# Performance work log

Measured on AMD Instinct MI355X. Metric: run time of the kernel, lower is better.

The kernel has to match this reference:

```python
import jax, jax.numpy as jnp
import numpy as np

B, S, IN, H, D, NH, L, C = 32, 512, 3, 64, 128, 8, 4, 5
NSUB = 10          # euler substeps per interval: dt = interval/10 for these inputs
MAX_CONSEC = 50    # max_consecutive_steps in torch code
DH = D // NH
EPS = 1e-5


def _ln(x, g, b):
    m = x.mean(-1, keepdims=True)
    v = ((x - m) ** 2).mean(-1, keepdims=True)
    return (x - m) / jnp.sqrt(v + EPS) * g + b


def setup_inputs():
    key = jax.random.key(0)
    ks = jax.random.split(key, 24)
    def g(i, shape, scale=0.05):
        return jax.random.normal(ks[i], shape, dtype=jnp.float32) * scale
    dts = jax.random.uniform(ks[0], (B, S), minval=0.001, maxval=0.05, dtype=jnp.float32)
    times = jnp.cumsum(dts, axis=1)  # strictly increasing, positive
    return dict(
        time_series=jax.random.normal(ks[1], (B, S, IN), dtype=jnp.float32),
        times=times,
        noise=jax.random.normal(ks[2], (S, NSUB, B, H), dtype=jnp.float32),
        mask=jnp.ones((B, S), dtype=bool),
        enc_w=g(3, (IN, H)), enc_b=jnp.zeros((H,)),
        enc_g=jnp.ones((H,)), enc_beta=jnp.zeros((H,)),
        dw1=g(4, (H + 1, 2 * H)), db1=jnp.zeros((2 * H,)),
        dw2=g(5, (2 * H, H)), db2=jnp.zeros((H,)),
        dw3=g(6, (H, H)), db3=jnp.zeros((H,)),
        aw1=g(7, (1, H)), ab1=jnp.zeros((H,)),
        aw2=g(8, (H, H)), ab2=jnp.zeros((H,)),
        bw1=g(9, (1, H)), bb1=jnp.zeros((H,)),
        bw2=g(10, (H, H)), bb2=jnp.zeros((H,)),
        min_diff=jnp.float32(0.1),
        in_w=g(11, (H, D)), in_b=jnp.zeros((D,)),
        wq=g(12, (L, D, D)), bq=jnp.zeros((L, D)),
        wk=g(13, (L, D, D)), bk=jnp.zeros((L, D)),
        wv=g(14, (L, D, D)), bv=jnp.zeros((L, D)),
        wo=g(15, (L, D, D)), bo=jnp.zeros((L, D)),
        ln1_g=jnp.ones((L, D)), ln1_b=jnp.zeros((L, D)),
        ln2_g=jnp.ones((L, D)), ln2_b=jnp.zeros((L, D)),
        fw1=g(16, (L, D, 4 * D)), fb1=jnp.zeros((L, 4 * D)),
        fw2=g(17, (L, 4 * D, D)), fb2=jnp.zeros((L, D)),
        cw1=g(18, (D, D // 2)), cb1=jnp.zeros((D // 2,)),
        cw2=g(19, (D // 2, C)), cb2=jnp.zeros((C,)),
    )


def reference(time_series, times, noise, mask, enc_w, enc_b, enc_g, enc_beta,
              dw1, db1, dw2, db2, dw3, db3, aw1, ab1, aw2, ab2, bw1, bb1, bw2, bb2,
              min_diff, in_w, in_b, wq, bq, wk, bk, wv, bv, wo, bo,
              ln1_g, ln1_b, ln2_g, ln2_b, fw1, fb1, fw2, fb2, cw1, cb1, cw2, cb2):
    # feature encoder: Linear -> LayerNorm -> ReLU (dropout off / eval)
    enc = jax.nn.relu(_ln(time_series @ enc_w + enc_b, enc_g, enc_beta))  # (B,S,H)

    def drift(t, y):
        tcol = jnp.full((y.shape[0], 1), t, dtype=y.dtype)
        ty = jnp.concatenate([y, tcol], axis=1)
        h1 = jnp.tanh(ty @ dw1 + db1)
        h2 = jnp.tanh(h1 @ dw2 + db2)
        return h2 @ dw3 + db3

    def diffusion(t, y):
        tcol = jnp.full((y.shape[0], 1), t, dtype=y.dtype)
        A = jax.nn.softplus(jnp.tanh(tcol @ aw1 + ab1) @ aw2 + ab2)
        Bt = jnp.tanh(jnp.tanh(tcol @ bw1 + bb1) @ bw2 + bb2)
        return A + Bt * y + jnp.abs(min_diff)

    t_seq = times[0]  # torch code uses batch element 0's timestamps for sdeint

    def step(carry, xs):
        state, consec = carry
        enc_i, t_prev, t_cur, dW = xs  # dW: (NSUB,B,H) standard normals
        h = (t_cur - t_prev) / NSUB    # dt = interval/10 (< self.dt for these inputs)
        sqh = jnp.sqrt(h)
        y0 = jax.lax.stop_gradient(state)  # torch detaches y0 at every step

        def sub(y, kw):
            k, dw = kw
            t = t_prev + k * h
            return y + drift(t, y) * h + diffusion(t, y) * sqh * dw, None

        y_int, _ = jax.lax.scan(sub, y0, (jnp.arange(NSUB, dtype=jnp.float32), dW))
        skip = consec >= MAX_CONSEC
        out = jnp.where(skip, enc_i, y_int)
        consec = jnp.where(skip, jnp.int32(0), consec + 1)
        return (out, consec), out

    y0 = enc[:, 0]
    xs = (jnp.swapaxes(enc, 0, 1)[1:], t_seq[:-1], t_seq[1:], noise[1:])
    _, traj = jax.lax.scan(step, (y0, jnp.int32(0)), xs)
    sde_features = jnp.concatenate([y0[:, None], jnp.swapaxes(traj, 0, 1)], axis=1)  # (B,S,H)

    mf = mask.astype(sde_features.dtype)
    sde_features = sde_features * mf[..., None]  # MaskedSequenceProcessor.apply_mask

    # ContiFormer (post-LN transformer encoder) over SDE features
    x = sde_features @ in_w + in_b  # (B,S,D)
    neg = jnp.asarray(-1e9, x.dtype)
    for l in range(L):
        q = (x @ wq[l] + bq[l]).reshape(B, S, NH, DH)
        k = (x @ wk[l] + bk[l]).reshape(B, S, NH, DH)
        v = (x @ wv[l] + bv[l]).reshape(B, S, NH, DH)
        scores = jnp.einsum('bqhd,bkhd->bhqk', q, k) / np.float32(np.sqrt(DH))
        scores = jnp.where(mask[:, None, None, :], scores, neg)
        att = jax.nn.softmax(scores, axis=-1)
        o = jnp.einsum('bhqk,bkhd->bqhd', att, v).reshape(B, S, D) @ wo[l] + bo[l]
        x = _ln(x + o, ln1_g[l], ln1_b[l])
        f = jax.nn.relu(x @ fw1[l] + fb1[l]) @ fw2[l] + fb2[l]
        x = _ln(x + f, ln2_g[l], ln2_b[l])
    pooled = (x * mf[..., None]).sum(1) / jnp.maximum(mf.sum(1, keepdims=True), 1.0)

    logits = jax.nn.relu(pooled @ cw1 + cb1) @ cw2 + cb2
    return logits, sde_features
```

## Files before the change

kernel.cpp:

```cpp
#include <hip/hip_runtime.h>
#include <hip/hip_bf16.h>


typedef __attribute__((ext_vector_type(8))) short short8;
typedef __attribute__((ext_vector_type(4))) float f32x4;

static constexpr int OFF_TS      = 0;
static constexpr int OFF_TIMES   = 49152;
static constexpr int OFF_ENCW    = 65536;
static constexpr int OFF_ENCB    = 65728;
static constexpr int OFF_ENCG    = 65792;
static constexpr int OFF_ENCBETA = 65856;
static constexpr int OFF_DW1     = 65920;
static constexpr int OFF_DB1     = 74240;
static constexpr int OFF_DW2     = 74368;
static constexpr int OFF_DB2     = 82560;
static constexpr int OFF_DW3     = 82624;
static constexpr int OFF_DB3     = 86720;
static constexpr int OFF_AW1     = 86784;
static constexpr int OFF_AB1     = 86848;
static constexpr int OFF_AW2     = 86912;
static constexpr int OFF_AB2     = 91008;
static constexpr int OFF_BW1     = 91072;
static constexpr int OFF_BB1     = 91136;
static constexpr int OFF_BW2     = 91200;
static constexpr int OFF_BB2     = 95296;
static constexpr int OFF_MD      = 95360;
static constexpr int OFF_INW     = 95424;
static constexpr int OFF_INB     = 103616;
static constexpr int OFF_WQ      = 103744;
static constexpr int OFF_BQ      = 169280;
static constexpr int OFF_WK      = 169792;
static constexpr int OFF_BK      = 235328;
static constexpr int OFF_WV      = 235840;
static constexpr int OFF_BV      = 301376;
static constexpr int OFF_WO      = 301888;
static constexpr int OFF_BO      = 367424;
static constexpr int OFF_LN1G    = 367936;
static constexpr int OFF_LN1B    = 368448;
static constexpr int OFF_LN2G    = 368960;
static constexpr int OFF_LN2B    = 369472;
static constexpr int OFF_FW1     = 369984;
static constexpr int OFF_FB1     = 632128;
static constexpr int OFF_FW2     = 634176;
static constexpr int OFF_FB2     = 896320;
static constexpr int OFF_CW1     = 896832;
static constexpr int OFF_CB1     = 905024;
static constexpr int OFF_CW2     = 905088;
static constexpr int OFF_CB2     = 905472;
static constexpr int OFF_FLAG    = 905536;
static constexpr int OFF_ENC     = 905600;
static constexpr int OFF_COEFA   = 3002752;
static constexpr int OFF_COEFB   = 3329792;
static constexpr int OFF_B1C     = 3656832;
static constexpr int OFF_X       = 4310912;
static constexpr int OFF_XBF     = 6408064;
static constexpr int OFF_QKVBF   = 7456640;
static constexpr int OFF_OBF     = 10602368;
static constexpr int OFF_HBF     = 11650944;
static constexpr int OFF_SDEBF   = 15845248;
static constexpr int OFF_WQKVT   = 16369536;
static constexpr int OFF_WOT     = 16467840;
static constexpr int OFF_FW1T    = 16500608;
static constexpr int OFF_FW2T    = 16631680;
static constexpr int OFF_INWT    = 16762752;
static constexpr int OFF_BQKV    = 16766848;
static constexpr int OFF_TMP     = 23185280;

struct PtrPack { const void* p[45]; };

__device__ inline float wsum64(float v) {
#pragma unroll
  for (int off = 32; off > 0; off >>= 1) v += __shfl_xor(v, off, 64);
  return v;
}

__device__ inline float fast_tanh(float x) {
  x = fminf(fmaxf(x, -15.f), 15.f);
  float e = __expf(2.f * x);
  return (e - 1.f) / (e + 1.f);
}

__device__ inline float tanh5(float x) {
  float e = __builtin_amdgcn_exp2f(x * 2.88539008f);
  return 1.f - 2.f * __builtin_amdgcn_rcpf(e + 1.f);
}

__device__ inline float bfdec(unsigned short h) {
  return __uint_as_float(((unsigned)h) << 16);
}

__device__ inline short f2bf(float f) {
  unsigned u = __float_as_uint(f);
  return (short)((u + 0x7FFFu + ((u >> 16) & 1u)) >> 16);
}

__device__ inline void lds_barrier() {
  asm volatile("s_waitcnt lgkmcnt(0)\ns_barrier" ::: "memory");
}

__global__ __launch_bounds__(256) void ingest_kernel(PtrPack pk, float* __restrict__ W) {
  const int NE = 43;
  const int cnt[NE] = {49152,16384,192,64,64,64,8320,128,8192,64,4096,64,64,64,4096,64,
                       64,64,4096,64,1,8192,128,65536,512,65536,512,65536,512,65536,512,
                       512,512,512,512,262144,2048,262144,512,8192,64,320,5};
  const int src[NE] = {0,1,4,5,6,7,8,9,10,11,12,13,14,15,16,17,18,19,20,21,22,23,24,
                       25,26,27,28,29,30,31,32,33,34,35,36,37,38,39,40,41,42,43,44};
  const int dst[NE] = {OFF_TS,OFF_TIMES,OFF_ENCW,OFF_ENCB,OFF_ENCG,OFF_ENCBETA,OFF_DW1,
                       OFF_DB1,OFF_DW2,OFF_DB2,OFF_DW3,OFF_DB3,OFF_AW1,OFF_AB1,OFF_AW2,
                       OFF_AB2,OFF_BW1,OFF_BB1,OFF_BW2,OFF_BB2,OFF_MD,OFF_INW,OFF_INB,
                       OFF_WQ,OFF_BQ,OFF_WK,OFF_BK,OFF_WV,OFF_BV,OFF_WO,OFF_BO,
                       OFF_LN1G,OFF_LN1B,OFF_LN2G,OFF_LN2B,OFF_FW1,OFF_FB1,OFF_FW2,
                       OFF_FB2,OFF_CW1,OFF_CB1,OFF_CW2,OFF_CB2};
  const unsigned* eg = (const unsigned*)pk.p[6];
  int gmode = (eg[0] == 0x3F803F80u) ? 1 : 0;

  __shared__ int isbf[NE];
  if (threadIdx.x < NE) {
    int k = threadIdx.x;
    int f = gmode;
    if (gmode) {
      const unsigned short* us = (const unsigned short*)pk.p[src[k]];
      int n = cnt[k] < 32 ? cnt[k] : 32;
      for (int i = 0; i < n; ++i) {
        unsigned short h = us[i];
        if (h & 0x7FFF) {
          float a = fabsf(bfdec(h));
          if (!(a > 1e-20f && a < 1e4f)) { f = 0; break; }
        }
      }
    }
    isbf[k] = f;
  }
  __syncthreads();

  int gid = blockIdx.x * 256 + threadIdx.x;
  int stride = gridDim.x * 256;
  if (gid == 0) {
    int nf = gmode;
    if (gmode) {
      const unsigned short* us = (const unsigned short*)pk.p[2];
      for (int i = 0; i < 32; ++i) {
        unsigned short h = us[i];
        if (h & 0x7FFF) {
          float a = fabsf(bfdec(h));
          if (!(a > 1e-20f && a < 1e4f)) { nf = 0; break; }
        }
      }
    }
    ((int*)W)[OFF_FLAG] = nf;
  }
  for (int k = 0; k < NE; ++k) {
    int n = cnt[k];
    float* dp = W + dst[k];
    if (isbf[k]) {
      const unsigned short* us = (const unsigned short*)pk.p[src[k]];
      for (int e = gid; e < n; e += stride) dp[e] = bfdec(us[e]);
    } else {
      const float* fs = (const float*)pk.p[src[k]];
      for (int e = gid; e < n; e += stride) dp[e] = fs[e];
    }
  }
}

__global__ __launch_bounds__(256) void prep_kernel(float* __restrict__ W) {
  short* wqkvT = (short*)(W + OFF_WQKVT);
  short* woT   = (short*)(W + OFF_WOT);
  short* fw1T  = (short*)(W + OFF_FW1T);
  short* fw2T  = (short*)(W + OFF_FW2T);
  short* inwT  = (short*)(W + OFF_INWT);
  float* bqkv  = W + OFF_BQKV;
  int gid = blockIdx.x * 256 + threadIdx.x;
  int stride = gridDim.x * 256;
  for (int e = gid; e < 796160; e += stride) {
    if (e < 196608) {
      int l = e / 49152, r = e % 49152, n = r >> 7, k = r & 127;
      float v = (n < 128) ? W[OFF_WQ + l*16384 + k*128 + n]
              : (n < 256) ? W[OFF_WK + l*16384 + k*128 + (n - 128)]
                          : W[OFF_WV + l*16384 + k*128 + (n - 256)];
      wqkvT[e] = f2bf(v);
    } else if (e < 262144) {
      int t = e - 196608; int l = t / 16384, r = t % 16384, n = r >> 7, k = r & 127;
      woT[t] = f2bf(W[OFF_WO + l*16384 + k*128 + n]);
    } else if (e < 524288) {
      int t = e - 262144; int l = t / 65536, r = t % 65536, n = r >> 7, k = r & 127;
      fw1T[t] = f2bf(W[OFF_FW1 + l*65536 + k*512 + n]);
    } else if (e < 786432) {
      int t = e - 524288; int l = t / 65536, r = t % 65536, n = r >> 9, k = r & 511;
      fw2T[t] = f2bf(W[OFF_FW2 + l*65536 + k*128 + n]);
    } else if (e < 794624) {
      int t = e - 786432; int n = t >> 6, k = t & 63;
      inwT[t] = f2bf(W[OFF_INW + k*128 + n]);
    } else {
      int t = e - 794624; int l = t / 384, j = t % 384;
      bqkv[t] = (j < 128) ? W[OFF_BQ + l*128 + j]
              : (j < 256) ? W[OFF_BK + l*128 + (j - 128)]
                          : W[OFF_BV + l*128 + (j - 256)];
    }
  }
}

__global__ __launch_bounds__(64) void encoder_kernel(float* __restrict__ W,
                                                     float* __restrict__ outf) {
  int row = blockIdx.x;
  int j = threadIdx.x;
  float t0 = W[OFF_TS + row*3 + 0];
  float t1 = W[OFF_TS + row*3 + 1];
  float t2 = W[OFF_TS + row*3 + 2];
  float v = W[OFF_ENCB + j] + t0 * W[OFF_ENCW + j] + t1 * W[OFF_ENCW + 64 + j]
          + t2 * W[OFF_ENCW + 128 + j];
  float mean = wsum64(v) * (1.f / 64.f);
  float d = v - mean;
  float var = wsum64(d * d) * (1.f / 64.f);
  float o = d * rsqrtf(var + 1e-5f) * W[OFF_ENCG + j] + W[OFF_ENCBETA + j];
  o = fmaxf(o, 0.f);
  W[OFF_ENC + row*64 + j] = o;
  int s = row & 511;
  if (s % 51 == 0) {
    ((short*)(W + OFF_SDEBF))[row*64 + j] = f2bf(o);
    outf[160 + row*64 + j] = o;
  }
}

__global__ __launch_bounds__(128) void precompute_kernel(float* __restrict__ W) {
  int bi = blockIdx.x;
  int step = bi / 10, k = bi - step * 10;
  float t_prev = W[OFF_TIMES + step];
  float t_cur  = W[OFF_TIMES + step + 1];
  float h = (t_cur - t_prev) * 0.1f;
  float t = t_prev + (float)k * h;
  __shared__ float av[64], bv[64];
  int tid = threadIdx.x;
  if (tid < 64) av[tid] = fast_tanh(t * W[OFF_AW1 + tid] + W[OFF_AB1 + tid]);
  else { int j = tid - 64; bv[j] = fast_tanh(t * W[OFF_BW1 + j] + W[OFF_BB1 + j]); }
  __syncthreads();
  if (tid < 64) {
    float a = W[OFF_AB2 + tid];
    for (int i = 0; i < 64; ++i) a += av[i] * W[OFF_AW2 + i*64 + tid];
    W[OFF_COEFA + bi*64 + tid] = fmaxf(a, 0.f) + log1pf(__expf(-fabsf(a)));
  } else {
    int j = tid - 64;
    float a = W[OFF_BB2 + j];
    for (int i = 0; i < 64; ++i) a += bv[i] * W[OFF_BW2 + i*64 + j];
    W[OFF_COEFB + bi*64 + j] = fast_tanh(a);
  }
  W[OFF_B1C + bi*128 + tid] = t * W[OFF_DW1 + 64*128 + tid] + W[OFF_DB1 + tid];
}

__global__ __launch_bounds__(256, 1) void sde_kernel(float* __restrict__ W,
                                                     const void* __restrict__ noise,
                                                     float* __restrict__ outf) {
  __shared__ short ybf[16 * 72];
  __shared__ short h1bf[16 * 136];
  __shared__ short h2bf[16 * 72];

  const int tid = threadIdx.x;
  const int w   = tid >> 6;
  const int lane = tid & 63;
  const int q   = lane >> 4;
  const int lq  = lane & 15;
  const int g   = blockIdx.x >> 1;
  const int r0  = (blockIdx.x & 1) * 16;

  const int nmode = ((const int*)W)[OFF_FLAG];
  const float md = fabsf(W[OFF_MD]);
  const unsigned short* nb16 = (const unsigned short*)noise;
  const float* nf32 = (const float*)noise;
  short* sdebf = (short*)(W + OFF_SDEBF);

  const int ncol = w*16 + lq;
  short8 B1f[2][2];
#pragma unroll
  for (int kt = 0; kt < 2; ++kt)
#pragma unroll
    for (int ct = 0; ct < 2; ++ct)
#pragma unroll
      for (int j = 0; j < 8; ++j)
        B1f[kt][ct][j] = f2bf(W[OFF_DW1 + (kt*32 + q*8 + j)*128 + w*32 + ct*16 + lq]);
  short8 B2f[4];
#pragma unroll
  for (int kt = 0; kt < 4; ++kt)
#pragma unroll
    for (int j = 0; j < 8; ++j)
      B2f[kt][j] = f2bf(W[OFF_DW2 + (kt*32 + q*8 + j)*64 + ncol]);
  short8 B3f[2];
#pragma unroll
  for (int kt = 0; kt < 2; ++kt)
#pragma unroll
    for (int j = 0; j < 8; ++j)
      B3f[kt][j] = f2bf(W[OFF_DW3 + (kt*32 + q*8 + j)*64 + ncol]);
  const float db2v = W[OFF_DB2 + ncol];
  const float db3v = W[OFF_DB3 + ncol];

  float yreg[4];
#pragma unroll
  for (int r = 0; r < 4; ++r) {
    yreg[r] = W[OFF_ENC + ((r0 + q*4 + r)*512 + 51*g)*64 + ncol];
    ybf[(q*4 + r)*72 + ncol] = f2bf(yreg[r]);
  }

  const int ci0 = 51*g*10;
  float bias_a = W[OFF_B1C + ci0*128 + w*32 + lq];
  float bias_b = W[OFF_B1C + ci0*128 + w*32 + 16 + lq];
  float ca = W[OFF_COEFA + ci0*64 + ncol];
  float cb = W[OFF_COEFB + ci0*64 + ncol];

  const int nsteps = (g == 10) ? 1 : 50;
  for (int m = 0; m < nsteps; ++m) {
    const int istep = 51*g + m;
    const float t_prev = W[OFF_TIMES + istep];
    const float t_cur  = W[OFF_TIMES + istep + 1];
    const float hstep = (t_cur - t_prev) * 0.1f;
    const float sqh = sqrtf(hstep);
    for (int k = 0; k < 10; ++k) {
      const int ci = istep*10 + k;
      const int cin = (ci + 1 > 5109) ? 5109 : ci + 1;
      float b1na = W[OFF_B1C + cin*128 + w*32 + lq];
      float b1nb = W[OFF_B1C + cin*128 + w*32 + 16 + lq];
      float can = W[OFF_COEFA + cin*64 + ncol];
      float cbn = W[OFF_COEFB + cin*64 + ncol];
      float dwv[4];
      {
        const int nb = (((istep + 1)*10 + k)*32 + r0 + q*4)*64 + ncol;
#pragma unroll
        for (int r = 0; r < 4; ++r)
          dwv[r] = nmode ? bfdec(nb16[nb + r*64]) : nf32[nb + r*64];
      }
      lds_barrier();
      {
        short8 a0 = *(const short8*)&ybf[lq*72 + q*8];
        short8 a1 = *(const short8*)&ybf[lq*72 + 32 + q*8];
        f32x4 c0 = {bias_a, bias_a, bias_a, bias_a};
        c0 = __builtin_amdgcn_mfma_f32_16x16x32_bf16(a0, B1f[0][0], c0, 0, 0, 0);
        c0 = __builtin_amdgcn_mfma_f32_16x16x32_bf16(a1, B1f[1][0], c0, 0, 0, 0);
        f32x4 c1 = {bias_b, bias_b, bias_b, bias_b};
        c1 = __builtin_amdgcn_mfma_f32_16x16x32_bf16(a0, B1f[0][1], c1, 0, 0, 0);
        c1 = __builtin_amdgcn_mfma_f32_16x16x32_bf16(a1, B1f[1][1], c1, 0, 0, 0);
#pragma unroll
        for (int r = 0; r < 4; ++r) {
          h1bf[(q*4 + r)*136 + w*32 + lq]      = f2bf(tanh5(c0[r]));
          h1bf[(q*4 + r)*136 + w*32 + 16 + lq] = f2bf(tanh5(c1[r]));
        }
      }
      lds_barrier();
      {
        short8 h0 = *(const short8*)&h1bf[lq*136 + q*8];
        short8 h1 = *(const short8*)&h1bf[lq*136 + 32 + q*8];
        short8 h2 = *(const short8*)&h1bf[lq*136 + 64 + q*8];
        short8 h3 = *(const short8*)&h1bf[lq*136 + 96 + q*8];
        f32x4 cA = {db2v, db2v, db2v, db2v};
        cA = __builtin_amdgcn_mfma_f32_16x16x32_bf16(h0, B2f[0], cA, 0, 0, 0);
        cA = __builtin_amdgcn_mfma_f32_16x16x32_bf16(h1, B2f[1], cA, 0, 0, 0);
        f32x4 cB = {0.f, 0.f, 0.f, 0.f};
        cB = __builtin_amdgcn_mfma_f32_16x16x32_bf16(h2, B2f[2], cB, 0, 0, 0);
        cB = __builtin_amdgcn_mfma_f32_16x16x32_bf16(h3, B2f[3], cB, 0, 0, 0);
#pragma unroll
        for (int r = 0; r < 4; ++r)
          h2bf[(q*4 + r)*72 + ncol] = f2bf(tanh5(cA[r] + cB[r]));
      }
      lds_barrier();
      {
        short8 g0 = *(const short8*)&h2bf[lq*72 + q*8];
        short8 g1 = *(const short8*)&h2bf[lq*72 + 32 + q*8];
        f32x4 d = {db3v, db3v, db3v, db3v};
        d = __builtin_amdgcn_mfma_f32_16x16x32_bf16(g0, B3f[0], d, 0, 0, 0);
        d = __builtin_amdgcn_mfma_f32_16x16x32_bf16(g1, B3f[1], d, 0, 0, 0);
#pragma unroll
        for (int r = 0; r < 4; ++r) {
          float yv = yreg[r];
          yv = yv + d[r]*hstep + (ca + cb*yv + md)*sqh*dwv[r];
          yreg[r] = yv;
          ybf[(q*4 + r)*72 + ncol] = f2bf(yv);
        }
      }
      bias_a = b1na; bias_b = b1nb; ca = can; cb = cbn;
    }
#pragma unroll
    for (int r = 0; r < 4; ++r) {
      const int gi = ((r0 + q*4 + r)*512 + (istep + 1))*64 + ncol;
      sdebf[gi] = f2bf(yreg[r]);
      outf[160 + gi] = yreg[r];
    }
  }
}

__global__ __launch_bounds__(256) void gemm_bf16_kernel(
    const short* __restrict__ A, const short* __restrict__ BT,
    const float* __restrict__ bias, float* __restrict__ Cf,
    short* __restrict__ Cb, int N, int K, int relu) {
  __shared__ short As[128 * 40];
  __shared__ short Bs[128 * 40];
  const int tid = threadIdx.x;
  const int w = tid >> 6, lane = tid & 63, q = lane >> 4, lq = lane & 15;
  const int wm = (w >> 1) * 64, wn = (w & 1) * 64;
  const int bm = blockIdx.x * 128, bn = blockIdx.y * 128;
  const int arow = tid >> 1, ah = (tid & 1) * 16;
  f32x4 acc[4][4];
#pragma unroll
  for (int i = 0; i < 4; ++i)
#pragma unroll
    for (int j = 0; j < 4; ++j) acc[i][j] = (f32x4){0.f, 0.f, 0.f, 0.f};

  for (int k0 = 0; k0 < K; k0 += 32) {
    short8 a0 = *(const short8*)&A[(bm + arow)*K + k0 + ah];
    short8 a1 = *(const short8*)&A[(bm + arow)*K + k0 + ah + 8];
    short8 b0 = *(const short8*)&BT[(bn + arow)*K + k0 + ah];
    short8 b1 = *(const short8*)&BT[(bn + arow)*K + k0 + ah + 8];
    __syncthreads();
    *(short8*)&As[arow*40 + ah]     = a0;
    *(short8*)&As[arow*40 + ah + 8] = a1;
    *(short8*)&Bs[arow*40 + ah]     = b0;
    *(short8*)&Bs[arow*40 + ah + 8] = b1;
    __syncthreads();
    short8 af[4], bf[4];
#pragma unroll
    for (int mi = 0; mi < 4; ++mi)
      af[mi] = *(const short8*)&As[(wm + mi*16 + lq)*40 + q*8];
#pragma unroll
    for (int ni = 0; ni < 4; ++ni)
      bf[ni] = *(const short8*)&Bs[(wn + ni*16 + lq)*40 + q*8];
#pragma unroll
    for (int mi = 0; mi < 4; ++mi)
#pragma unroll
      for (int ni = 0; ni < 4; ++ni)
        acc[mi][ni] = __builtin_amdgcn_mfma_f32_16x16x32_bf16(af[mi], bf[ni],
                                                              acc[mi][ni], 0, 0, 0);
  }
#pragma unroll
  for (int ni = 0; ni < 4; ++ni) {
    const int col = bn + wn + ni*16 + lq;
    const float bv = bias ? bias[col] : 0.f;
#pragma unroll
    for (int mi = 0; mi < 4; ++mi) {
#pragma unroll
      for (int r = 0; r < 4; ++r) {
        const int row = bm + wm + mi*16 + q*4 + r;
        float v = acc[mi][ni][r] + bv;
        if (relu) v = fmaxf(v, 0.f);
        if (Cf) Cf[row*N + col] = v;
        if (Cb) Cb[row*N + col] = f2bf(v);
      }
    }
  }
}

__global__ __launch_bounds__(256) void gemm_ln64_kernel(
    const short* __restrict__ A, const short* __restrict__ BT,
    const float* __restrict__ bias, float* __restrict__ X,
    short* __restrict__ Xb, int K,
    const float* __restrict__ lng, const float* __restrict__ lnb) {
  __shared__ short As[64 * 40];
  __shared__ short Bs[128 * 40];
  const int tid = threadIdx.x;
  const int w = tid >> 6, lane = tid & 63, q = lane >> 4, lq = lane & 15;
  const int bm = blockIdx.x * 64;
  f32x4 acc[8];
#pragma unroll
  for (int i = 0; i < 8; ++i) acc[i] = (f32x4){0.f, 0.f, 0.f, 0.f};

  const int arow = tid >> 2, acol = (tid & 3) * 8;
  const int brow = tid >> 1, bcol = (tid & 1) * 16;
  for (int k0 = 0; k0 < K; k0 += 32) {
    short8 a  = *(const short8*)&A[(bm + arow)*K + k0 + acol];
    short8 b0 = *(const short8*)&BT[brow*K + k0 + bcol];
    short8 b1 = *(const short8*)&BT[brow*K + k0 + bcol + 8];
    __syncthreads();
    *(short8*)&As[arow*40 + acol]    = a;
    *(short8*)&Bs[brow*40 + bcol]    = b0;
    *(short8*)&Bs[brow*40 + bcol+8]  = b1;
    __syncthreads();
    short8 af = *(const short8*)&As[(w*16 + lq)*40 + q*8];
#pragma unroll
    for (int ni = 0; ni < 8; ++ni) {
      short8 bf = *(const short8*)&Bs[(ni*16 + lq)*40 + q*8];
      acc[ni] = __builtin_amdgcn_mfma_f32_16x16x32_bf16(af, bf, acc[ni], 0, 0, 0);
    }
  }
  if (lng == nullptr) {
#pragma unroll
    for (int r = 0; r < 4; ++r) {
      const int row = bm + w*16 + q*4 + r;
#pragma unroll
      for (int ni = 0; ni < 8; ++ni) {
        const int col = ni*16 + lq;
        float v = acc[ni][r] + bias[col];
        X[row*128 + col] = v;
        Xb[row*128 + col] = f2bf(v);
      }
    }
  } else {
#pragma unroll
    for (int r = 0; r < 4; ++r) {
      const int row = bm + w*16 + q*4 + r;
      float v[8];
      float s = 0.f, s2 = 0.f;
#pragma unroll
      for (int ni = 0; ni < 8; ++ni) {
        const int col = ni*16 + lq;
        float t = acc[ni][r] + bias[col] + X[row*128 + col];
        v[ni] = t; s += t; s2 += t*t;
      }
#pragma unroll
      for (int off = 1; off < 16; off <<= 1) {
        s  += __shfl_xor(s, off, 16);
        s2 += __shfl_xor(s2, off, 16);
      }
      float mean = s * (1.f / 128.f);
      float var = s2 * (1.f / 128.f) - mean * mean;
      float inv = rsqrtf(var + 1e-5f);
#pragma unroll
      for (int ni = 0; ni < 8; ++ni) {
        const int col = ni*16 + lq;
        float o = (v[ni] - mean) * inv * lng[col] + lnb[col];
        X[row*128 + col] = o;
        Xb[row*128 + col] = f2bf(o);
      }
    }
  }
}

__global__ __launch_bounds__(256) void attn_kernel(const short* __restrict__ QKV,
                                                   short* __restrict__ O) {
  __shared__ short Kt[512 * 20];
  __shared__ short Vt[16 * 520];
  __shared__ short Pb[4 * 16 * 136];
  const int blk = blockIdx.x;
  const int h = blk & 7, b = blk >> 3;
  const int tid = threadIdx.x;
  const int w = tid >> 6, lane = tid & 63, q = lane >> 4, lq = lane & 15;

#pragma unroll
  for (int kk = 0; kk < 2; ++kk) {
    const int key = tid + kk*256;
    const short* src = &QKV[(size_t)(b*512 + key)*384 + 128 + h*16];
    short8 k0 = *(const short8*)src;
    short8 k1 = *(const short8*)(src + 8);
    *(short8*)&Kt[key*20]     = k0;
    *(short8*)&Kt[key*20 + 8] = k1;
    short8 v0 = *(const short8*)(src + 128);
    short8 v1 = *(const short8*)(src + 136);
#pragma unroll
    for (int d = 0; d < 8; ++d) Vt[d*520 + key] = v0[d];
#pragma unroll
    for (int d = 0; d < 8; ++d) Vt[(8 + d)*520 + key] = v1[d];
  }
  __syncthreads();

  short* Pw = &Pb[w * 2176];
  const float cexp = 0.25f * 1.44269504f;

  for (int qi = 0; qi < 8; ++qi) {
    const int qrow0 = b*512 + (w*8 + qi)*16;
    short8 aq = (short8){0,0,0,0,0,0,0,0};
    if (q < 2) aq = *(const short8*)&QKV[(size_t)(qrow0 + lq)*384 + h*16 + q*8];

    f32x4 acc[32];
#pragma unroll
    for (int t = 0; t < 32; ++t) {
      short8 bk = (short8){0,0,0,0,0,0,0,0};
      if (q < 2) bk = *(const short8*)&Kt[(t*16 + lq)*20 + q*8];
      f32x4 z = {0.f, 0.f, 0.f, 0.f};
      acc[t] = __builtin_amdgcn_mfma_f32_16x16x32_bf16(aq, bk, z, 0, 0, 0);
    }
    float mx[4] = {-1e30f, -1e30f, -1e30f, -1e30f};
#pragma unroll
    for (int t = 0; t < 32; ++t)
#pragma unroll
      for (int r = 0; r < 4; ++r) mx[r] = fmaxf(mx[r], acc[t][r]);
#pragma unroll
    for (int off = 1; off < 16; off <<= 1)
#pragma unroll
      for (int r = 0; r < 4; ++r) mx[r] = fmaxf(mx[r], __shfl_xor(mx[r], off, 16));
    float ls[4] = {0.f, 0.f, 0.f, 0.f};
#pragma unroll
    for (int t = 0; t < 32; ++t)
#pragma unroll
      for (int r = 0; r < 4; ++r) {
        float p = __builtin_amdgcn_exp2f((acc[t][r] - mx[r]) * cexp);
        acc[t][r] = p;
        ls[r] += p;
      }
#pragma unroll
    for (int off = 1; off < 16; off <<= 1)
#pragma unroll
      for (int r = 0; r < 4; ++r) ls[r] += __shfl_xor(ls[r], off, 16);

    f32x4 o = {0.f, 0.f, 0.f, 0.f};
#pragma unroll
    for (int c = 0; c < 4; ++c) {
#pragma unroll
      for (int tt = 0; tt < 8; ++tt)
#pragma unroll
        for (int r = 0; r < 4; ++r)
          Pw[(q*4 + r)*136 + tt*16 + lq] =
              (short)(__float_as_uint(acc[c*8 + tt][r]) >> 16);
#pragma unroll
      for (int kk = 0; kk < 4; ++kk) {
        short8 ap = *(const short8*)&Pw[lq*136 + kk*32 + q*8];
        short8 bv = *(const short8*)&Vt[lq*520 + c*128 + kk*32 + q*8];
        o = __builtin_amdgcn_mfma_f32_16x16x32_bf16(ap, bv, o, 0, 0, 0);
      }
    }
#pragma unroll
    for (int r = 0; r < 4; ++r) {
      float ov = o[r] * __builtin_amdgcn_rcpf(ls[r]);
      O[(size_t)(qrow0 + q*4 + r)*128 + h*16 + lq] = f2bf(ov);
    }
  }
}

__global__ __launch_bounds__(128) void pool_cls_kernel(const float* __restrict__ W,
                                                       float* __restrict__ outf) {
  int b = blockIdx.x, j = threadIdx.x;
  float s0 = 0.f, s1 = 0.f, s2 = 0.f, s3 = 0.f;
  const float* xb = W + OFF_X + b*512*128 + j;
  for (int ss = 0; ss < 128; ++ss) {
    s0 += xb[ss*128];
    s1 += xb[(128 + ss)*128];
    s2 += xb[(256 + ss)*128];
    s3 += xb[(384 + ss)*128];
  }
  __shared__ float pooled[128];
  __shared__ float hid[64];
  pooled[j] = (s0 + s1 + s2 + s3) * (1.f / 512.f);
  __syncthreads();
  if (j < 64) {
    float a = W[OFF_CB1 + j];
    for (int i = 0; i < 128; ++i) a += pooled[i] * W[OFF_CW1 + i*64 + j];
    hid[j] = fmaxf(a, 0.f);
  }
  __syncthreads();
  if (j < 5) {
    float a = W[OFF_CB2 + j];
    for (int i = 0; i < 64; ++i) a += hid[i] * W[OFF_CW2 + i*5 + j];
    outf[b*5 + j] = a;
  }
}

extern "C" void kernel_launch(void* const* d_in, const int* in_sizes, int n_in,
                              void* d_out, int out_size, void* d_ws, size_t ws_size,
                              hipStream_t stream) {
  (void)in_sizes; (void)out_size; (void)ws_size;
  float* W = reinterpret_cast<float*>(d_ws);
  float* outf = reinterpret_cast<float*>(d_out);
  short* sdebf = (short*)(W + OFF_SDEBF);
  short* xbf   = (short*)(W + OFF_XBF);
  short* qkvbf = (short*)(W + OFF_QKVBF);
  short* obf   = (short*)(W + OFF_OBF);
  short* hbf   = (short*)(W + OFF_HBF);
  PtrPack pk;
  for (int i = 0; i < 45 && i < n_in; ++i) pk.p[i] = d_in[i];

  ingest_kernel<<<512, 256, 0, stream>>>(pk, W);
  prep_kernel<<<512, 256, 0, stream>>>(W);
  encoder_kernel<<<16384, 64, 0, stream>>>(W, outf);
  precompute_kernel<<<5110, 128, 0, stream>>>(W);
  sde_kernel<<<22, 256, 0, stream>>>(W, d_in[2], outf);

  gemm_ln64_kernel<<<256, 256, 0, stream>>>(sdebf, (short*)(W + OFF_INWT),
      W + OFF_INB, W + OFF_X, xbf, 64, nullptr, nullptr);
  for (int l = 0; l < 4; ++l) {
    gemm_bf16_kernel<<<dim3(128, 3), 256, 0, stream>>>(xbf,
        (short*)(W + OFF_WQKVT) + l*49152, W + OFF_BQKV + l*384,
        (float*)nullptr, qkvbf, 384, 128, 0);
    attn_kernel<<<256, 256, 0, stream>>>(qkvbf, obf);
    gemm_ln64_kernel<<<256, 256, 0, stream>>>(obf,
        (short*)(W + OFF_WOT) + l*16384, W + OFF_BO + l*128,
        W + OFF_X, xbf, 128, W + OFF_LN1G + l*128, W + OFF_LN1B + l*128);
    gemm_bf16_kernel<<<dim3(128, 4), 256, 0, stream>>>(xbf,
        (short*)(W + OFF_FW1T) + l*65536, W + OFF_FB1 + l*512,
        (float*)nullptr, hbf, 512, 128, 1);
    gemm_ln64_kernel<<<256, 256, 0, stream>>>(hbf,
        (short*)(W + OFF_FW2T) + l*65536, W + OFF_FB2 + l*128,
        W + OFF_X, xbf, 512, W + OFF_LN2G + l*128, W + OFF_LN2B + l*128);
  }
  pool_cls_kernel<<<32, 128, 0, stream>>>(W, outf);
}
```

Baseline: 1.026 ms.

## Fuse transformer stages into one persistent kernel with grid barriers

Replaces the 21 separate transformer GEMM, attention and LayerNorm launches with one persistent 256-block kernel. The stages are separated by atomic grid barriers whose counters are reset in the ingest kernel. The prep, encoder and precompute kernels are also merged into a single setup kernel that splits its blocks by role. The aim is to remove per-launch overhead and tail gaps between small kernels, at the cost of spin-wait barriers and a co-residency requirement: all 256 blocks must be resident at once, or the kernel deadlocks.

```diff
diff --git a/kernel.cpp b/kernel.cpp
--- a/kernel.cpp
+++ b/kernel.cpp
@@ -65,7 +65,7 @@
 static constexpr int OFF_FW2T    = 16631680;
 static constexpr int OFF_INWT    = 16762752;
 static constexpr int OFF_BQKV    = 16766848;
-static constexpr int OFF_TMP     = 23185280;
+static constexpr int OFF_BAR     = 23185280;
 
 struct PtrPack { const void* p[45]; };
 
@@ -97,6 +97,25 @@
 
 __device__ inline void lds_barrier() {
   asm volatile("s_waitcnt lgkmcnt(0)\ns_barrier" ::: "memory");
+}
+
+__device__ inline void grid_barrier(unsigned* bar, int id) {
+  __syncthreads();
+  if (threadIdx.x == 0) {
+    __threadfence();
+    unsigned old = __hip_atomic_fetch_add(&bar[id], 1u, __ATOMIC_ACQ_REL,
+                                          __HIP_MEMORY_SCOPE_AGENT);
+    if (old == 255u) {
+      __hip_atomic_store(&bar[64 + id], 1u, __ATOMIC_RELEASE,
+                         __HIP_MEMORY_SCOPE_AGENT);
+    } else {
+      while (!__hip_atomic_load(&bar[64 + id], __ATOMIC_ACQUIRE,
+                                __HIP_MEMORY_SCOPE_AGENT))
+        __builtin_amdgcn_s_sleep(8);
+    }
+    __threadfence();
+  }
+  __syncthreads();
 }
 
 __global__ __launch_bounds__(256) void ingest_kernel(PtrPack pk, float* __restrict__ W) {
@@ -136,6 +155,7 @@
 
   int gid = blockIdx.x * 256 + threadIdx.x;
   int stride = gridDim.x * 256;
+  if (gid < 128) ((unsigned*)(W + OFF_BAR))[gid] = 0u;
   if (gid == 0) {
     int nf = gmode;
     if (gmode) {
@@ -163,88 +183,99 @@
   }
 }
 
-__global__ __launch_bounds__(256) void prep_kernel(float* __restrict__ W) {
-  short* wqkvT = (short*)(W + OFF_WQKVT);
-  short* woT   = (short*)(W + OFF_WOT);
-  short* fw1T  = (short*)(W + OFF_FW1T);
-  short* fw2T  = (short*)(W + OFF_FW2T);
-  short* inwT  = (short*)(W + OFF_INWT);
-  float* bqkv  = W + OFF_BQKV;
-  int gid = blockIdx.x * 256 + threadIdx.x;
-  int stride = gridDim.x * 256;
-  for (int e = gid; e < 796160; e += stride) {
-    if (e < 196608) {
-      int l = e / 49152, r = e % 49152, n = r >> 7, k = r & 127;
-      float v = (n < 128) ? W[OFF_WQ + l*16384 + k*128 + n]
-              : (n < 256) ? W[OFF_WK + l*16384 + k*128 + (n - 128)]
-                          : W[OFF_WV + l*16384 + k*128 + (n - 256)];
-      wqkvT[e] = f2bf(v);
-    } else if (e < 262144) {
-      int t = e - 196608; int l = t / 16384, r = t % 16384, n = r >> 7, k = r & 127;
-      woT[t] = f2bf(W[OFF_WO + l*16384 + k*128 + n]);
-    } else if (e < 524288) {
-      int t = e - 262144; int l = t / 65536, r = t % 65536, n = r >> 7, k = r & 127;
-      fw1T[t] = f2bf(W[OFF_FW1 + l*65536 + k*512 + n]);
-    } else if (e < 786432) {
-      int t = e - 524288; int l = t / 65536, r = t % 65536, n = r >> 9, k = r & 511;
-      fw2T[t] = f2bf(W[OFF_FW2 + l*65536 + k*128 + n]);
-    } else if (e < 794624) {
-      int t = e - 786432; int n = t >> 6, k = t & 63;
-      inwT[t] = f2bf(W[OFF_INW + k*128 + n]);
-    } else {
-      int t = e - 794624; int l = t / 384, j = t % 384;
-      bqkv[t] = (j < 128) ? W[OFF_BQ + l*128 + j]
-              : (j < 256) ? W[OFF_BK + l*128 + (j - 128)]
-                          : W[OFF_BV + l*128 + (j - 256)];
-    }
-  }
-}
-
-__global__ __launch_bounds__(64) void encoder_kernel(float* __restrict__ W,
+__global__ __launch_bounds__(256) void setup2_kernel(float* __restrict__ W,
                                                      float* __restrict__ outf) {
-  int row = blockIdx.x;
-  int j = threadIdx.x;
-  float t0 = W[OFF_TS + row*3 + 0];
-  float t1 = W[OFF_TS + row*3 + 1];
-  float t2 = W[OFF_TS + row*3 + 2];
-  float v = W[OFF_ENCB + j] + t0 * W[OFF_ENCW + j] + t1 * W[OFF_ENCW + 64 + j]
-          + t2 * W[OFF_ENCW + 128 + j];
-  float mean = wsum64(v) * (1.f / 64.f);
-  float d = v - mean;
-  float var = wsum64(d * d) * (1.f / 64.f);
-  float o = d * rsqrtf(var + 1e-5f) * W[OFF_ENCG + j] + W[OFF_ENCBETA + j];
-  o = fmaxf(o, 0.f);
-  W[OFF_ENC + row*64 + j] = o;
-  int s = row & 511;
-  if (s % 51 == 0) {
-    ((short*)(W + OFF_SDEBF))[row*64 + j] = f2bf(o);
-    outf[160 + row*64 + j] = o;
-  }
-}
-
-__global__ __launch_bounds__(128) void precompute_kernel(float* __restrict__ W) {
-  int bi = blockIdx.x;
-  int step = bi / 10, k = bi - step * 10;
-  float t_prev = W[OFF_TIMES + step];
-  float t_cur  = W[OFF_TIMES + step + 1];
-  float h = (t_cur - t_prev) * 0.1f;
-  float t = t_prev + (float)k * h;
-  __shared__ float av[64], bv[64];
-  int tid = threadIdx.x;
-  if (tid < 64) av[tid] = fast_tanh(t * W[OFF_AW1 + tid] + W[OFF_AB1 + tid]);
-  else { int j = tid - 64; bv[j] = fast_tanh(t * W[OFF_BW1 + j] + W[OFF_BB1 + j]); }
-  __syncthreads();
-  if (tid < 64) {
-    float a = W[OFF_AB2 + tid];
-    for (int i = 0; i < 64; ++i) a += av[i] * W[OFF_AW2 + i*64 + tid];
-    W[OFF_COEFA + bi*64 + tid] = fmaxf(a, 0.f) + log1pf(__expf(-fabsf(a)));
+  const int bid = blockIdx.x;
+  const int tid = threadIdx.x;
+  __shared__ float av2[2][64], bv2[2][64];
+
+  if (bid < 128) {
+    short* wqkvT = (short*)(W + OFF_WQKVT);
+    short* woT   = (short*)(W + OFF_WOT);
+    short* fw1T  = (short*)(W + OFF_FW1T);
+    short* fw2T  = (short*)(W + OFF_FW2T);
+    short* inwT  = (short*)(W + OFF_INWT);
+    float* bqkv  = W + OFF_BQKV;
+    int gid = bid * 256 + tid;
+    int stride = 128 * 256;
+    for (int e = gid; e < 796160; e += stride) {
+      if (e < 196608) {
+        int l = e / 49152, r = e % 49152, n = r >> 7, k = r & 127;
+        float v = (n < 128) ? W[OFF_WQ + l*16384 + k*128 + n]
+                : (n < 256) ? W[OFF_WK + l*16384 + k*128 + (n - 128)]
+                            : W[OFF_WV + l*16384 + k*128 + (n - 256)];
+        wqkvT[e] = f2bf(v);
+      } else if (e < 262144) {
+        int t = e - 196608; int l = t / 16384, r = t % 16384, n = r >> 7, k = r & 127;
+        woT[t] = f2bf(W[OFF_WO + l*16384 + k*128 + n]);
+      } else if (e < 524288) {
+        int t = e - 262144; int l = t / 65536, r = t % 65536, n = r >> 7, k = r & 127;
+        fw1T[t] = f2bf(W[OFF_FW1 + l*65536 + k*512 + n]);
+      } else if (e < 786432) {
+        int t = e - 524288; int l = t / 65536, r = t % 65536, n = r >> 9, k = r & 511;
+        fw2T[t] = f2bf(W[OFF_FW2 + l*65536 + k*128 + n]);
+      } else if (e < 794624) {
+        int t = e - 786432; int n = t >> 6, k = t & 63;
+        inwT[t] = f2bf(W[OFF_INW + k*128 + n]);
+      } else {
+        int t = e - 794624; int l = t / 384, j = t % 384;
+        bqkv[t] = (j < 128) ? W[OFF_BQ + l*128 + j]
+                : (j < 256) ? W[OFF_BK + l*128 + (j - 128)]
+                            : W[OFF_BV + l*128 + (j - 256)];
+      }
+    }
+  } else if (bid < 768) {
+    int w = tid >> 6, j = tid & 63;
+    for (int row = (bid - 128)*4 + w; row < 16384; row += 640*4) {
+      float t0 = W[OFF_TS + row*3 + 0];
+      float t1 = W[OFF_TS + row*3 + 1];
+      float t2 = W[OFF_TS + row*3 + 2];
+      float v = W[OFF_ENCB + j] + t0 * W[OFF_ENCW + j] + t1 * W[OFF_ENCW + 64 + j]
+              + t2 * W[OFF_ENCW + 128 + j];
+      float mean = wsum64(v) * (1.f / 64.f);
+      float d = v - mean;
+      float var = wsum64(d * d) * (1.f / 64.f);
+      float o = d * rsqrtf(var + 1e-5f) * W[OFF_ENCG + j] + W[OFF_ENCBETA + j];
+      o = fmaxf(o, 0.f);
+      W[OFF_ENC + row*64 + j] = o;
+      int s = row & 511;
+      if (s % 51 == 0) {
+        ((short*)(W + OFF_SDEBF))[row*64 + j] = f2bf(o);
+        outf[160 + row*64 + j] = o;
+      }
+    }
   } else {
-    int j = tid - 64;
-    float a = W[OFF_BB2 + j];
-    for (int i = 0; i < 64; ++i) a += bv[i] * W[OFF_BW2 + i*64 + j];
-    W[OFF_COEFB + bi*64 + j] = fast_tanh(a);
-  }
-  W[OFF_B1C + bi*128 + tid] = t * W[OFF_DW1 + 64*128 + tid] + W[OFF_DB1 + tid];
+    int half = tid >> 7, lt = tid & 127;
+    for (int base = (bid - 768)*2; base < 5110; base += 1024) {
+      int bi = base + half;
+      bool act = bi < 5110;
+      float t = 0.f;
+      if (act) {
+        int step = bi / 10, k = bi - step * 10;
+        float t_prev = W[OFF_TIMES + step];
+        float t_cur  = W[OFF_TIMES + step + 1];
+        float h = (t_cur - t_prev) * 0.1f;
+        t = t_prev + (float)k * h;
+        if (lt < 64) av2[half][lt] = fast_tanh(t * W[OFF_AW1 + lt] + W[OFF_AB1 + lt]);
+        else { int j = lt - 64; bv2[half][j] = fast_tanh(t * W[OFF_BW1 + j] + W[OFF_BB1 + j]); }
+      }
+      __syncthreads();
+      if (act) {
+        if (lt < 64) {
+          float a = W[OFF_AB2 + lt];
+          for (int i = 0; i < 64; ++i) a += av2[half][i] * W[OFF_AW2 + i*64 + lt];
+          W[OFF_COEFA + bi*64 + lt] = fmaxf(a, 0.f) + log1pf(__expf(-fabsf(a)));
+        } else {
+          int j = lt - 64;
+          float a = W[OFF_BB2 + j];
+          for (int i = 0; i < 64; ++i) a += bv2[half][i] * W[OFF_BW2 + i*64 + j];
+          W[OFF_COEFB + bi*64 + j] = fast_tanh(a);
+        }
+        W[OFF_B1C + bi*128 + lt] = t * W[OFF_DW1 + 64*128 + lt] + W[OFF_DB1 + lt];
+      }
+      __syncthreads();
+    }
+  }
 }
 
 __global__ __launch_bounds__(256, 1) void sde_kernel(float* __restrict__ W,
@@ -384,16 +415,16 @@
   }
 }
 
-__global__ __launch_bounds__(256) void gemm_bf16_kernel(
-    const short* __restrict__ A, const short* __restrict__ BT,
-    const float* __restrict__ bias, float* __restrict__ Cf,
-    short* __restrict__ Cb, int N, int K, int relu) {
-  __shared__ short As[128 * 40];
-  __shared__ short Bs[128 * 40];
+
+__device__ void gemm128_job(const short* __restrict__ A, const short* __restrict__ BT,
+                            const float* __restrict__ bias, short* __restrict__ Cb,
+                            int N, int K, int relu, int bm, int bn,
+                            short* __restrict__ sm) {
+  short* As = sm;
+  short* Bs = sm + 128*40;
   const int tid = threadIdx.x;
   const int w = tid >> 6, lane = tid & 63, q = lane >> 4, lq = lane & 15;
   const int wm = (w >> 1) * 64, wn = (w & 1) * 64;
-  const int bm = blockIdx.x * 128, bn = blockIdx.y * 128;
   const int arow = tid >> 1, ah = (tid & 1) * 16;
   f32x4 acc[4][4];
 #pragma unroll
@@ -437,23 +468,22 @@
         const int row = bm + wm + mi*16 + q*4 + r;
         float v = acc[mi][ni][r] + bv;
         if (relu) v = fmaxf(v, 0.f);
-        if (Cf) Cf[row*N + col] = v;
-        if (Cb) Cb[row*N + col] = f2bf(v);
-      }
-    }
-  }
-}
-
-__global__ __launch_bounds__(256) void gemm_ln64_kernel(
-    const short* __restrict__ A, const short* __restrict__ BT,
-    const float* __restrict__ bias, float* __restrict__ X,
-    short* __restrict__ Xb, int K,
-    const float* __restrict__ lng, const float* __restrict__ lnb) {
-  __shared__ short As[64 * 40];
-  __shared__ short Bs[128 * 40];
+        Cb[row*N + col] = f2bf(v);
+      }
+    }
+  }
+}
+
+__device__ void ln64_job(const short* __restrict__ A, const short* __restrict__ BT,
+                         const float* __restrict__ bias, float* __restrict__ X,
+                         short* __restrict__ Xb, int K,
+                         const float* __restrict__ lng, const float* __restrict__ lnb,
+                         int bid, short* __restrict__ sm) {
+  short* As = sm;
+  short* Bs = sm + 64*40;
   const int tid = threadIdx.x;
   const int w = tid >> 6, lane = tid & 63, q = lane >> 4, lq = lane & 15;
-  const int bm = blockIdx.x * 64;
+  const int bm = bid * 64;
   f32x4 acc[8];
 #pragma unroll
   for (int i = 0; i < 8; ++i) acc[i] = (f32x4){0.f, 0.f, 0.f, 0.f};
@@ -519,13 +549,12 @@
   }
 }
 
-__global__ __launch_bounds__(256) void attn_kernel(const short* __restrict__ QKV,
-                                                   short* __restrict__ O) {
-  __shared__ short Kt[512 * 20];
-  __shared__ short Vt[16 * 520];
-  __shared__ short Pb[4 * 16 * 136];
-  const int blk = blockIdx.x;
-  const int h = blk & 7, b = blk >> 3;
+__device__ void attn_job(const short* __restrict__ QKV, short* __restrict__ O,
+                         int bid, short* __restrict__ sm) {
+  short* Kt = sm;
+  short* Vt = sm + 10240;
+  short* Pb = sm + 18560;
+  const int h = bid & 7, b = bid >> 3;
   const int tid = threadIdx.x;
   const int w = tid >> 6, lane = tid & 63, q = lane >> 4, lq = lane & 15;
 
@@ -609,20 +638,22 @@
   }
 }
 
-__global__ __launch_bounds__(128) void pool_cls_kernel(const float* __restrict__ W,
-                                                       float* __restrict__ outf) {
-  int b = blockIdx.x, j = threadIdx.x;
-  float s0 = 0.f, s1 = 0.f, s2 = 0.f, s3 = 0.f;
-  const float* xb = W + OFF_X + b*512*128 + j;
-  for (int ss = 0; ss < 128; ++ss) {
-    s0 += xb[ss*128];
-    s1 += xb[(128 + ss)*128];
-    s2 += xb[(256 + ss)*128];
-    s3 += xb[(384 + ss)*128];
-  }
-  __shared__ float pooled[128];
-  __shared__ float hid[64];
-  pooled[j] = (s0 + s1 + s2 + s3) * (1.f / 512.f);
+__device__ void pool_job(const float* __restrict__ W, float* __restrict__ outf,
+                         int b, float* __restrict__ psm) {
+  const int j = threadIdx.x;
+  float* pooled = psm;
+  float* hid = psm + 128;
+  if (j < 128) {
+    float s0 = 0.f, s1 = 0.f, s2 = 0.f, s3 = 0.f;
+    const float* xb = W + OFF_X + b*512*128 + j;
+    for (int ss = 0; ss < 128; ++ss) {
+      s0 += xb[ss*128];
+      s1 += xb[(128 + ss)*128];
+      s2 += xb[(256 + ss)*128];
+      s3 += xb[(384 + ss)*128];
+    }
+    pooled[j] = (s0 + s1 + s2 + s3) * (1.f / 512.f);
+  }
   __syncthreads();
   if (j < 64) {
     float a = W[OFF_CB1 + j];
@@ -635,6 +666,46 @@
     for (int i = 0; i < 64; ++i) a += hid[i] * W[OFF_CW2 + i*5 + j];
     outf[b*5 + j] = a;
   }
+}
+
+__global__ __launch_bounds__(256, 2) void trans_kernel(float* __restrict__ W,
+                                                       float* __restrict__ outf) {
+  __shared__ __align__(16) short sm[27264];
+  unsigned* bar = (unsigned*)(W + OFF_BAR);
+  const int bid = blockIdx.x;
+
+  short* sdebf = (short*)(W + OFF_SDEBF);
+  short* xbf   = (short*)(W + OFF_XBF);
+  short* qkvbf = (short*)(W + OFF_QKVBF);
+  short* obf   = (short*)(W + OFF_OBF);
+  short* hbf   = (short*)(W + OFF_HBF);
+
+  ln64_job(sdebf, (short*)(W + OFF_INWT), W + OFF_INB, W + OFF_X, xbf, 64,
+           nullptr, nullptr, bid, sm);
+  grid_barrier(bar, 0);
+
+  for (int l = 0; l < 4; ++l) {
+    for (int j = bid; j < 384; j += 256)
+      gemm128_job(xbf, (short*)(W + OFF_WQKVT) + l*49152, W + OFF_BQKV + l*384,
+                  qkvbf, 384, 128, 0, (j & 127)*128, (j >> 7)*128, sm);
+    grid_barrier(bar, 1 + l*5);
+    attn_job(qkvbf, obf, bid, sm);
+    grid_barrier(bar, 2 + l*5);
+    ln64_job(obf, (short*)(W + OFF_WOT) + l*16384, W + OFF_BO + l*128,
+             W + OFF_X, xbf, 128, W + OFF_LN1G + l*128, W + OFF_LN1B + l*128,
+             bid, sm);
+    grid_barrier(bar, 3 + l*5);
+    for (int j = bid; j < 512; j += 256)
+      gemm128_job(xbf, (short*)(W + OFF_FW1T) + l*65536, W + OFF_FB1 + l*512,
+                  hbf, 512, 128, 1, (j & 127)*128, (j >> 7)*128, sm);
+    grid_barrier(bar, 4 + l*5);
+    ln64_job(hbf, (short*)(W + OFF_FW2T) + l*65536, W + OFF_FB2 + l*128,
+             W + OFF_X, xbf, 512, W + OFF_LN2G + l*128, W + OFF_LN2B + l*128,
+             bid, sm);
+    grid_barrier(bar, 5 + l*5);
+  }
+
+  if (bid < 32) pool_job(W, outf, bid, (float*)sm);
 }
 
 extern "C" void kernel_launch(void* const* d_in, const int* in_sizes, int n_in,
@@ -643,36 +714,11 @@
   (void)in_sizes; (void)out_size; (void)ws_size;
   float* W = reinterpret_cast<float*>(d_ws);
   float* outf = reinterpret_cast<float*>(d_out);
-  short* sdebf = (short*)(W + OFF_SDEBF);
-  short* xbf   = (short*)(W + OFF_XBF);
-  short* qkvbf = (short*)(W + OFF_QKVBF);
-  short* obf   = (short*)(W + OFF_OBF);
-  short* hbf   = (short*)(W + OFF_HBF);
   PtrPack pk;
   for (int i = 0; i < 45 && i < n_in; ++i) pk.p[i] = d_in[i];
 
   ingest_kernel<<<512, 256, 0, stream>>>(pk, W);
-  prep_kernel<<<512, 256, 0, stream>>>(W);
-  encoder_kernel<<<16384, 64, 0, stream>>>(W, outf);
-  precompute_kernel<<<5110, 128, 0, stream>>>(W);
+  setup2_kernel<<<1280, 256, 0, stream>>>(W, outf);
   sde_kernel<<<22, 256, 0, stream>>>(W, d_in[2], outf);
-
-  gemm_ln64_kernel<<<256, 256, 0, stream>>>(sdebf, (short*)(W + OFF_INWT),
-      W + OFF_INB, W + OFF_X, xbf, 64, nullptr, nullptr);
-  for (int l = 0; l < 4; ++l) {
-    gemm_bf16_kernel<<<dim3(128, 3), 256, 0, stream>>>(xbf,
-        (short*)(W + OFF_WQKVT) + l*49152, W + OFF_BQKV + l*384,
-        (float*)nullptr, qkvbf, 384, 128, 0);
-    attn_kernel<<<256, 256, 0, stream>>>(qkvbf, obf);
-    gemm_ln64_kernel<<<256, 256, 0, stream>>>(obf,
-        (short*)(W + OFF_WOT) + l*16384, W + OFF_BO + l*128,
-        W + OFF_X, xbf, 128, W + OFF_LN1G + l*128, W + OFF_LN1B + l*128);
-    gemm_bf16_kernel<<<dim3(128, 4), 256, 0, stream>>>(xbf,
-        (short*)(W + OFF_FW1T) + l*65536, W + OFF_FB1 + l*512,
-        (float*)nullptr, hbf, 512, 128, 1);
-    gemm_ln64_kernel<<<256, 256, 0, stream>>>(hbf,
-        (short*)(W + OFF_FW2T) + l*65536, W + OFF_FB2 + l*128,
-        W + OFF_X, xbf, 512, W + OFF_LN2G + l*128, W + OFF_LN2B + l*128);
-  }
-  pool_cls_kernel<<<32, 128, 0, stream>>>(W, outf);
-}
+  trans_kernel<<<256, 256, 0, stream>>>(W, outf);
+}
```

New measurement: 1.720 ms. 1.68x slower.
